# Performance work log

Measured on AMD Instinct MI355X. Metric: run time of the kernel, lower is better.

The kernel has to match this reference:

```python
import jax, jax.numpy as jnp
import numpy as np

IN_DIM = 256
QK_DIM = IN_DIM // 8


def setup_inputs() -> dict:
    key = jax.random.key(0)
    ks = jax.random.split(key, 7)
    B, C, H, W = 4, IN_DIM, 64, 64
    s = 0.05
    return {
        "x": jax.random.normal(ks[0], (B, C, H, W), dtype=jnp.float32),
        "Wq": jax.random.normal(ks[1], (QK_DIM, C), dtype=jnp.float32) * s,
        "bq": jnp.zeros((QK_DIM,), dtype=jnp.float32),
        "Wk": jax.random.normal(ks[2], (QK_DIM, C), dtype=jnp.float32) * s,
        "bk": jnp.zeros((QK_DIM,), dtype=jnp.float32),
        "Wv": jax.random.normal(ks[3], (C, C), dtype=jnp.float32) * s,
        "bv": jnp.zeros((C,), dtype=jnp.float32),
        "gamma": jnp.zeros((1,), dtype=jnp.float32),
    }


def reference(x, Wq, bq, Wk, bk, Wv, bv, gamma):
    B, C, H, W = x.shape
    N = H * W
    xf = x.reshape(B, C, N)  # [B, C, N]
    # 1x1 convs are channel matmuls
    q = jnp.einsum('oc,bcn->bno', Wq, xf) + bq  # [B, N, Cqk]
    k = jnp.einsum('oc,bcn->bon', Wk, xf) + bk[None, :, None]  # [B, Cqk, N]
    energy = jnp.einsum('bno,bom->bnm', q, k)  # [B, N, N]
    attn = jax.nn.softmax(energy, axis=-1)
    v = jnp.einsum('oc,bcn->bon', Wv, xf) + bv[None, :, None]  # [B, C, N]
    # torch: out = bmm(v, attn^T) -> out[b,c,m] = sum_n v[b,c,n]*attn[m,n]
    out = jnp.einsum('bcn,bmn->bcm', v, attn)
    out = out.reshape(B, C, H, W)
    return gamma[0] * out + x
```

## Files before the change

### kernel.cpp

```cpp
#include <hip/hip_runtime.h>
#include <hip/hip_bf16.h>
#include <cstddef>

#define NB  4
#define NC  256
#define NN  4096
#define DQK 32
#define MT  64
#define JT  64
#define NIT (NN / JT)
#define XS2 264

typedef __attribute__((ext_vector_type(8))) short short8;
typedef __attribute__((ext_vector_type(4))) float f32x4;

#define MFMA16(a, b, c) __builtin_amdgcn_mfma_f32_16x16x32_bf16((a), (b), (c), 0, 0, 0)

__device__ inline unsigned pk2bf(float a, float b) {
  __hip_bfloat162 h = __float22bfloat162_rn(make_float2(a, b));
  unsigned u;
  __builtin_memcpy(&u, &h, 4);
  return u;
}

__device__ inline void gl16(const void* g, void* s) {
  __builtin_amdgcn_global_load_lds(
      (const __attribute__((address_space(1))) void*)g,
      (__attribute__((address_space(3))) void*)s, 16, 0, 0);
}

template <int N>
__device__ inline void bar_vm() {
  asm volatile("s_waitcnt lgkmcnt(0)" ::: "memory");
  asm volatile("s_waitcnt vmcnt(%0)" ::"n"(N) : "memory");
  __builtin_amdgcn_s_barrier();
  asm volatile("" ::: "memory");
}

__global__ __launch_bounds__(256) void wcvt_kernel(
    const float* __restrict__ Wq, const float* __restrict__ Wk,
    const float* __restrict__ Wv, __hip_bfloat16* __restrict__ W16) {
  const int id4 = (blockIdx.x * 256 + threadIdx.x) * 4;
  const int row = id4 >> 8, col = id4 & 255;
  const float* src = (row < 32) ? Wq + row * 256
                   : (row < 64) ? Wk + (row - 32) * 256
                                : Wv + (row - 64) * 256;
  float4 vv = *(const float4*)(src + col);
  *(uint2*)(W16 + id4) = make_uint2(pk2bf(vv.x, vv.y), pk2bf(vv.z, vv.w));
}

__global__ __launch_bounds__(256, 4) void proj_kernel(
    const float* __restrict__ x, const __hip_bfloat16* __restrict__ W16,
    const float* __restrict__ bq, const float* __restrict__ bk,
    const float* __restrict__ bv, __hip_bfloat16* __restrict__ q,
    __hip_bfloat16* __restrict__ kT, __hip_bfloat16* __restrict__ v) {
  __shared__ __hip_bfloat16 Xs[32 * XS2];
  const int t = threadIdx.x;
  const int b = blockIdx.y, n0 = blockIdx.x * 32;
  const int w = __builtin_amdgcn_readfirstlane(t >> 6);
  const int ln = t & 15, quad = (t & 63) >> 4;
  const int sn = t & 31, scg = t >> 5;

  const float* xsrc = x + (size_t)b * NC * NN + n0 + sn;
#pragma unroll
  for (int g = 0; g < 4; ++g) {
    float xr[8];
#pragma unroll
    for (int i = 0; i < 8; ++i)
      xr[i] = xsrc[(size_t)(g * 64 + scg * 8 + i) * NN];
    uint4 pw;
    pw.x = pk2bf(xr[0], xr[1]);
    pw.y = pk2bf(xr[2], xr[3]);
    pw.z = pk2bf(xr[4], xr[5]);
    pw.w = pk2bf(xr[6], xr[7]);
    *(uint4*)&Xs[sn * XS2 + g * 64 + scg * 8] = pw;
  }
  __syncthreads();

  f32x4 zero4 = {0.f, 0.f, 0.f, 0.f};
  f32x4 acc[5][2];
#pragma unroll
  for (int i = 0; i < 5; ++i)
#pragma unroll
    for (int j = 0; j < 2; ++j) acc[i][j] = zero4;

  const __hip_bfloat16* wbase = W16 + (size_t)(w * 80 + ln) * NC + quad * 8;
  short8 afc[5], afn[5];
#pragma unroll
  for (int ot = 0; ot < 5; ++ot)
    afc[ot] = *(const short8*)(wbase + (size_t)ot * 16 * NC);

#pragma unroll 1
  for (int k0 = 0; k0 < NC; k0 += 32) {
    const int kn = k0 + 32;
    if (kn < NC) {
#pragma unroll
      for (int ot = 0; ot < 5; ++ot)
        afn[ot] = *(const short8*)(wbase + (size_t)ot * 16 * NC + kn);
    }
    short8 bfr[2];
#pragma unroll
    for (int nt = 0; nt < 2; ++nt)
      bfr[nt] = *(const short8*)&Xs[(nt * 16 + ln) * XS2 + k0 + quad * 8];
#pragma unroll
    for (int ot = 0; ot < 5; ++ot)
#pragma unroll
      for (int nt = 0; nt < 2; ++nt)
        acc[ot][nt] = MFMA16(afc[ot], bfr[nt], acc[ot][nt]);
#pragma unroll
    for (int ot = 0; ot < 5; ++ot) afc[ot] = afn[ot];
  }

#pragma unroll
  for (int ot = 0; ot < 5; ++ot) {
    const int gbase = w * 80 + ot * 16;
    if (gbase < 32) {
#pragma unroll
      for (int nt = 0; nt < 2; ++nt)
#pragma unroll
        for (int r = 0; r < 4; ++r) {
          const int row = gbase + quad * 4 + r;
          q[((size_t)b * NN + n0 + nt * 16 + ln) * DQK + row] =
              __hip_bfloat16(acc[ot][nt][r] + bq[row]);
        }
    } else if (gbase < 64) {
#pragma unroll
      for (int nt = 0; nt < 2; ++nt)
#pragma unroll
        for (int r = 0; r < 4; ++r) {
          const int row = gbase - 32 + quad * 4 + r;
          kT[((size_t)b * NN + n0 + nt * 16 + ln) * DQK + row] =
              __hip_bfloat16(acc[ot][nt][r] + bk[row]);
        }
    } else {
#pragma unroll
      for (int nt = 0; nt < 2; ++nt)
#pragma unroll
        for (int r = 0; r < 4; ++r) {
          const int c = gbase - 64 + quad * 4 + r;
          v[((size_t)b * NC + c) * NN + n0 + nt * 16 + ln] =
              __hip_bfloat16(acc[ot][nt][r] + bv[c]);
        }
    }
  }
}

__global__ __launch_bounds__(512, 2) void flash_kernel(
    const __hip_bfloat16* __restrict__ q, const __hip_bfloat16* __restrict__ kt,
    const __hip_bfloat16* __restrict__ v, const float* __restrict__ x,
    const float* __restrict__ gamma, float* __restrict__ out) {
  __shared__ __align__(16) __hip_bfloat16 Vs[4][NC * JT];
  __shared__ __align__(16) __hip_bfloat16 Ks[3][JT * DQK];
  __shared__ __align__(16) __hip_bfloat16 Ps[2][MT * JT];
  __shared__ float lrow[MT];

  const int t  = threadIdx.x;
  const int bi = blockIdx.x;
  const int b  = (bi & 7) >> 1;
  const int m0 = (((bi & 1) * 32) + (bi >> 3)) * MT;

  const int w    = __builtin_amdgcn_readfirstlane(t >> 6);
  const int l    = t & 63;
  const int ln   = t & 15;
  const int quad = (t & 63) >> 4;

  const __hip_bfloat16* kb_base = kt + (size_t)b * NN * DQK;
  const __hip_bfloat16* v_base  = v + (size_t)b * NC * NN;

  size_t voff[4];
#pragma unroll
  for (int k = 0; k < 4; ++k)
    voff[k] = (size_t)((w * 4 + k) * 8 + (l >> 3)) * NN +
              (((l & 7) ^ ((l >> 3) & 7)) * 8);
  const size_t koff = (size_t)(w * 16 + (l >> 2)) * DQK +
                      (((l & 3) ^ ((l >> 2) & 3)) * 8);

#pragma unroll
  for (int j = 0; j < 2; ++j) {
#pragma unroll
    for (int k = 0; k < 4; ++k)
      gl16(v_base + voff[k] + (size_t)j * JT, &Vs[j][(w * 4 + k) * 512]);
    if (w < 4)
      gl16(kb_base + koff + (size_t)j * JT * DQK, &Ks[j][w * 512]);
  }

  if (w < 4) {
    bar_vm<5>();
    const short8 qa =
        *(const short8*)(q + ((size_t)b * NN + m0 + w * 16 + ln) * DQK + quad * 8);
    float lreg = 0.f;
    const f32x4 zero4 = {0.f, 0.f, 0.f, 0.f};
    const int m = w * 16 + ln;

    for (int it = 0; it < NIT; ++it) {
      const bool more = (it + 2 < NIT);
      if (more) {
        const size_t jn = (size_t)(it + 2) * JT;
#pragma unroll
        for (int k = 0; k < 4; ++k)
          gl16(v_base + voff[k] + jn, &Vs[(it + 2) & 3][(w * 4 + k) * 512]);
        gl16(kb_base + koff + jn * DQK, &Ks[(it + 2) % 3][w * 512]);
      }

      short8 kb[4];
#pragma unroll
      for (int jt = 0; jt < 4; ++jt)
        kb[jt] = *(const short8*)&Ks[it % 3][(jt * 16 + ln) * DQK +
                                             ((quad ^ (ln & 3)) * 8)];
      f32x4 st[4];
      __builtin_amdgcn_s_setprio(1);
#pragma unroll
      for (int jt = 0; jt < 4; ++jt) st[jt] = MFMA16(kb[jt], qa, zero4);
      __builtin_amdgcn_s_setprio(0);

      char* pbase = (char*)&Ps[it & 1][0] + m * (JT * 2);
#pragma unroll
      for (int jt = 0; jt < 4; ++jt) {
        const float e0 = __expf(st[jt][0]), e1 = __expf(st[jt][1]);
        const float e2 = __expf(st[jt][2]), e3 = __expf(st[jt][3]);
        lreg += (e0 + e1) + (e2 + e3);
        *(uint2*)(pbase + ((jt * 32 + quad * 8) ^ ((m & 7) << 4))) =
            make_uint2(pk2bf(e0, e1), pk2bf(e2, e3));
      }
      if (more) bar_vm<5>(); else bar_vm<0>();
    }
    lreg += __shfl_xor(lreg, 16);
    lreg += __shfl_xor(lreg, 32);
    if (quad == 0) lrow[m] = lreg;
    __syncthreads();
  } else {
    bar_vm<8>();
    const int c0 = (w - 4) * 64;
    const f32x4 zero4 = {0.f, 0.f, 0.f, 0.f};
    f32x4 acc[4][4];
#pragma unroll
    for (int ct = 0; ct < 4; ++ct)
#pragma unroll
      for (int mt = 0; mt < 4; ++mt) acc[ct][mt] = zero4;

    for (int it = 0; it < NIT; ++it) {
      const bool more = (it + 2 < NIT);
      if (more) {
        const size_t jn = (size_t)(it + 2) * JT;
#pragma unroll
        for (int k = 0; k < 4; ++k)
          gl16(v_base + voff[k] + jn, &Vs[(it + 2) & 3][(w * 4 + k) * 512]);
      }
      if (it > 0) {
        const char* vbb = (const char*)&Vs[(it - 1) & 3][0];
        const char* pbb = (const char*)&Ps[(it - 1) & 1][0];
        short8 va[4][2];
#pragma unroll
        for (int ct = 0; ct < 4; ++ct)
#pragma unroll
          for (int ks = 0; ks < 2; ++ks)
            va[ct][ks] = *(const short8*)(vbb +
                (size_t)(c0 + ct * 16 + ln) * (JT * 2) +
                (((ks * 4 + quad) ^ (ln & 7)) * 16));
#pragma unroll
        for (int ks = 0; ks < 2; ++ks) {
          short8 pb[4];
#pragma unroll
          for (int mt = 0; mt < 4; ++mt)
            pb[mt] = *(const short8*)(pbb + (size_t)(mt * 16 + ln) * (JT * 2) +
                                      ((ks * 64 + quad * 16) ^ ((ln & 7) << 4)));
          __builtin_amdgcn_s_setprio(1);
#pragma unroll
          for (int ct = 0; ct < 4; ++ct)
#pragma unroll
            for (int mt = 0; mt < 4; ++mt)
              acc[ct][mt] = MFMA16(va[ct][ks], pb[mt], acc[ct][mt]);
          __builtin_amdgcn_s_setprio(0);
        }
      }
      if (more) bar_vm<8>(); else bar_vm<0>();
    }

    {
      const char* vbb = (const char*)&Vs[(NIT - 1) & 3][0];
      const char* pbb = (const char*)&Ps[(NIT - 1) & 1][0];
      short8 va[4][2];
#pragma unroll
      for (int ct = 0; ct < 4; ++ct)
#pragma unroll
        for (int ks = 0; ks < 2; ++ks)
          va[ct][ks] = *(const short8*)(vbb +
              (size_t)(c0 + ct * 16 + ln) * (JT * 2) +
              (((ks * 4 + quad) ^ (ln & 7)) * 16));
#pragma unroll
      for (int ks = 0; ks < 2; ++ks) {
        short8 pb[4];
#pragma unroll
        for (int mt = 0; mt < 4; ++mt)
          pb[mt] = *(const short8*)(pbb + (size_t)(mt * 16 + ln) * (JT * 2) +
                                    ((ks * 64 + quad * 16) ^ ((ln & 7) << 4)));
        __builtin_amdgcn_s_setprio(1);
#pragma unroll
        for (int ct = 0; ct < 4; ++ct)
#pragma unroll
          for (int mt = 0; mt < 4; ++mt)
            acc[ct][mt] = MFMA16(va[ct][ks], pb[mt], acc[ct][mt]);
        __builtin_amdgcn_s_setprio(0);
      }
    }
    __syncthreads();

    const float g0 = gamma[0];
    float li[4];
#pragma unroll
    for (int mt = 0; mt < 4; ++mt) li[mt] = 1.f / lrow[mt * 16 + ln];
#pragma unroll
    for (int ct = 0; ct < 4; ++ct)
#pragma unroll
      for (int r = 0; r < 4; ++r) {
        const int c = c0 + ct * 16 + quad * 4 + r;
        const float* xr = x + ((size_t)b * NC + c) * NN + m0;
        float* orow = out + ((size_t)b * NC + c) * NN + m0;
#pragma unroll
        for (int mt = 0; mt < 4; ++mt) {
          const int m = mt * 16 + ln;
          orow[m] = g0 * (acc[ct][mt][r] * li[mt]) + xr[m];
        }
      }
  }
}

extern "C" void kernel_launch(void* const* d_in, const int* in_sizes, int n_in,
                              void* d_out, int out_size, void* d_ws, size_t ws_size,
                              hipStream_t stream) {
  const float* x     = (const float*)d_in[0];
  const float* Wq    = (const float*)d_in[1];
  const float* bq    = (const float*)d_in[2];
  const float* Wk    = (const float*)d_in[3];
  const float* bk    = (const float*)d_in[4];
  const float* Wv    = (const float*)d_in[5];
  const float* bv    = (const float*)d_in[6];
  const float* gamma = (const float*)d_in[7];
  float* out = (float*)d_out;

  char* wsp = (char*)d_ws;
  __hip_bfloat16* W16 = (__hip_bfloat16*)wsp;  wsp += (size_t)320 * NC * 2;
  __hip_bfloat16* q   = (__hip_bfloat16*)wsp;  wsp += (size_t)NB * NN * DQK * 2;
  __hip_bfloat16* kT  = (__hip_bfloat16*)wsp;  wsp += (size_t)NB * NN * DQK * 2;
  __hip_bfloat16* v   = (__hip_bfloat16*)wsp;

  wcvt_kernel<<<dim3(80), dim3(256), 0, stream>>>(Wq, Wk, Wv, W16);
  proj_kernel<<<dim3(NN / 32, NB), dim3(256), 0, stream>>>(x, W16, bq, bk, bv, q, kT, v);
  flash_kernel<<<dim3(NB * NN / MT), dim3(512), 0, stream>>>(q, kT, v, x, gamma, out);
}
```

Before: 162.7 us.

## Replace producer/consumer warp specialization with symmetric split-K over key halves

Instead of 4 waves computing QK^T/exp and 4 waves doing the PV matmul, all 8 waves now do both: each wave owns a channel quarter and one half of each 64-key tile. Partial PV accumulators from the two key halves are reduced through shared memory (reusing the V buffer) at the end, and the row sums are combined from two halves. This is meant to remove the idle imbalance of the specialized wave roles and spread the exp work across all waves. The cost is an extra cross-wave reduction, a duplicated small QK^T MFMA per wave pair, and different barrier counts per wave group.

```diff
diff --git a/kernel.cpp b/kernel.cpp
--- a/kernel.cpp
+++ b/kernel.cpp
@@ -151,8 +151,8 @@
     const float* __restrict__ gamma, float* __restrict__ out) {
   __shared__ __align__(16) __hip_bfloat16 Vs[4][NC * JT];
   __shared__ __align__(16) __hip_bfloat16 Ks[3][JT * DQK];
-  __shared__ __align__(16) __hip_bfloat16 Ps[2][MT * JT];
-  __shared__ float lrow[MT];
+  __shared__ __align__(16) __hip_bfloat16 Ps[2][2][MT * 32];
+  __shared__ float lrow[2][MT];
 
   const int t  = threadIdx.x;
   const int bi = blockIdx.x;
@@ -163,6 +163,8 @@
   const int l    = t & 63;
   const int ln   = t & 15;
   const int quad = (t & 63) >> 4;
+  const int cq   = w & 3;
+  const int jh   = w >> 2;
 
   const __hip_bfloat16* kb_base = kt + (size_t)b * NN * DQK;
   const __hip_bfloat16* v_base  = v + (size_t)b * NC * NN;
@@ -172,7 +174,7 @@
   for (int k = 0; k < 4; ++k)
     voff[k] = (size_t)((w * 4 + k) * 8 + (l >> 3)) * NN +
               (((l & 7) ^ ((l >> 3) & 7)) * 8);
-  const size_t koff = (size_t)(w * 16 + (l >> 2)) * DQK +
+  const size_t koff = (size_t)(cq * 16 + (l >> 2)) * DQK +
                       (((l & 3) ^ ((l >> 2) & 3)) * 8);
 
 #pragma unroll
@@ -180,146 +182,142 @@
 #pragma unroll
     for (int k = 0; k < 4; ++k)
       gl16(v_base + voff[k] + (size_t)j * JT, &Vs[j][(w * 4 + k) * 512]);
-    if (w < 4)
-      gl16(kb_base + koff + (size_t)j * JT * DQK, &Ks[j][w * 512]);
-  }
-
-  if (w < 4) {
-    bar_vm<5>();
-    const short8 qa =
-        *(const short8*)(q + ((size_t)b * NN + m0 + w * 16 + ln) * DQK + quad * 8);
-    float lreg = 0.f;
-    const f32x4 zero4 = {0.f, 0.f, 0.f, 0.f};
-    const int m = w * 16 + ln;
-
-    for (int it = 0; it < NIT; ++it) {
-      const bool more = (it + 2 < NIT);
-      if (more) {
-        const size_t jn = (size_t)(it + 2) * JT;
-#pragma unroll
-        for (int k = 0; k < 4; ++k)
-          gl16(v_base + voff[k] + jn, &Vs[(it + 2) & 3][(w * 4 + k) * 512]);
-        gl16(kb_base + koff + jn * DQK, &Ks[(it + 2) % 3][w * 512]);
-      }
-
-      short8 kb[4];
-#pragma unroll
-      for (int jt = 0; jt < 4; ++jt)
-        kb[jt] = *(const short8*)&Ks[it % 3][(jt * 16 + ln) * DQK +
-                                             ((quad ^ (ln & 3)) * 8)];
-      f32x4 st[4];
+    if (jh == 0)
+      gl16(kb_base + koff + (size_t)j * JT * DQK, &Ks[j][cq * 512]);
+  }
+  if (jh == 0) bar_vm<5>(); else bar_vm<4>();
+
+  const short8 qa =
+      *(const short8*)(q + ((size_t)b * NN + m0 + cq * 16 + ln) * DQK + quad * 8);
+  const f32x4 zero4 = {0.f, 0.f, 0.f, 0.f};
+  float lreg = 0.f;
+  const int m  = cq * 16 + ln;
+  const int fp = (ln >> 1) & 3;
+  f32x4 acc[4][4];
+#pragma unroll
+  for (int ct = 0; ct < 4; ++ct)
+#pragma unroll
+    for (int mt = 0; mt < 4; ++mt) acc[ct][mt] = zero4;
+
+  for (int it = 0; it < NIT; ++it) {
+    const bool more = (it + 2 < NIT);
+    if (more) {
+      const size_t jn = (size_t)(it + 2) * JT;
+#pragma unroll
+      for (int k = 0; k < 4; ++k)
+        gl16(v_base + voff[k] + jn, &Vs[(it + 2) & 3][(w * 4 + k) * 512]);
+      if (jh == 0)
+        gl16(kb_base + koff + jn * DQK, &Ks[(it + 2) % 3][cq * 512]);
+    }
+
+    short8 kb[2];
+#pragma unroll
+    for (int jt = 0; jt < 2; ++jt) {
+      const int row = jh * 32 + jt * 16 + ln;
+      kb[jt] = *(const short8*)&Ks[it % 3][row * DQK + ((quad ^ (ln & 3)) * 8)];
+    }
+    f32x4 st[2];
+    __builtin_amdgcn_s_setprio(1);
+#pragma unroll
+    for (int jt = 0; jt < 2; ++jt) st[jt] = MFMA16(kb[jt], qa, zero4);
+    __builtin_amdgcn_s_setprio(0);
+
+    char* prow = (char*)&Ps[it & 1][jh][0] + m * 64;
+#pragma unroll
+    for (int jt = 0; jt < 2; ++jt) {
+      const float e0 = __expf(st[jt][0]), e1 = __expf(st[jt][1]);
+      const float e2 = __expf(st[jt][2]), e3 = __expf(st[jt][3]);
+      lreg += (e0 + e1) + (e2 + e3);
+      *(uint2*)(prow + (((jt * 2 + (quad >> 1)) ^ fp) * 16) + (quad & 1) * 8) =
+          make_uint2(pk2bf(e0, e1), pk2bf(e2, e3));
+    }
+
+    if (it > 0) {
+      const char* vbb = (const char*)&Vs[(it - 1) & 3][0];
+      const char* pbb = (const char*)&Ps[(it - 1) & 1][jh][0];
+      short8 va[4], pb[4];
+#pragma unroll
+      for (int ct = 0; ct < 4; ++ct)
+        va[ct] = *(const short8*)(vbb + (size_t)(cq * 64 + ct * 16 + ln) * 128 +
+                                  (((jh * 4 + quad) ^ (ln & 7)) * 16));
+#pragma unroll
+      for (int mt = 0; mt < 4; ++mt)
+        pb[mt] = *(const short8*)(pbb + (size_t)(mt * 16 + ln) * 64 +
+                                  ((quad ^ fp) * 16));
       __builtin_amdgcn_s_setprio(1);
 #pragma unroll
-      for (int jt = 0; jt < 4; ++jt) st[jt] = MFMA16(kb[jt], qa, zero4);
+      for (int ct = 0; ct < 4; ++ct)
+#pragma unroll
+        for (int mt = 0; mt < 4; ++mt)
+          acc[ct][mt] = MFMA16(va[ct], pb[mt], acc[ct][mt]);
       __builtin_amdgcn_s_setprio(0);
-
-      char* pbase = (char*)&Ps[it & 1][0] + m * (JT * 2);
-#pragma unroll
-      for (int jt = 0; jt < 4; ++jt) {
-        const float e0 = __expf(st[jt][0]), e1 = __expf(st[jt][1]);
-        const float e2 = __expf(st[jt][2]), e3 = __expf(st[jt][3]);
-        lreg += (e0 + e1) + (e2 + e3);
-        *(uint2*)(pbase + ((jt * 32 + quad * 8) ^ ((m & 7) << 4))) =
-            make_uint2(pk2bf(e0, e1), pk2bf(e2, e3));
-      }
-      if (more) bar_vm<5>(); else bar_vm<0>();
-    }
-    lreg += __shfl_xor(lreg, 16);
-    lreg += __shfl_xor(lreg, 32);
-    if (quad == 0) lrow[m] = lreg;
-    __syncthreads();
-  } else {
-    bar_vm<8>();
-    const int c0 = (w - 4) * 64;
-    const f32x4 zero4 = {0.f, 0.f, 0.f, 0.f};
-    f32x4 acc[4][4];
-#pragma unroll
-    for (int ct = 0; ct < 4; ++ct)
-#pragma unroll
-      for (int mt = 0; mt < 4; ++mt) acc[ct][mt] = zero4;
-
-    for (int it = 0; it < NIT; ++it) {
-      const bool more = (it + 2 < NIT);
-      if (more) {
-        const size_t jn = (size_t)(it + 2) * JT;
-#pragma unroll
-        for (int k = 0; k < 4; ++k)
-          gl16(v_base + voff[k] + jn, &Vs[(it + 2) & 3][(w * 4 + k) * 512]);
-      }
-      if (it > 0) {
-        const char* vbb = (const char*)&Vs[(it - 1) & 3][0];
-        const char* pbb = (const char*)&Ps[(it - 1) & 1][0];
-        short8 va[4][2];
-#pragma unroll
-        for (int ct = 0; ct < 4; ++ct)
-#pragma unroll
-          for (int ks = 0; ks < 2; ++ks)
-            va[ct][ks] = *(const short8*)(vbb +
-                (size_t)(c0 + ct * 16 + ln) * (JT * 2) +
-                (((ks * 4 + quad) ^ (ln & 7)) * 16));
-#pragma unroll
-        for (int ks = 0; ks < 2; ++ks) {
-          short8 pb[4];
-#pragma unroll
-          for (int mt = 0; mt < 4; ++mt)
-            pb[mt] = *(const short8*)(pbb + (size_t)(mt * 16 + ln) * (JT * 2) +
-                                      ((ks * 64 + quad * 16) ^ ((ln & 7) << 4)));
-          __builtin_amdgcn_s_setprio(1);
-#pragma unroll
-          for (int ct = 0; ct < 4; ++ct)
-#pragma unroll
-            for (int mt = 0; mt < 4; ++mt)
-              acc[ct][mt] = MFMA16(va[ct][ks], pb[mt], acc[ct][mt]);
-          __builtin_amdgcn_s_setprio(0);
-        }
-      }
-      if (more) bar_vm<8>(); else bar_vm<0>();
-    }
-
-    {
-      const char* vbb = (const char*)&Vs[(NIT - 1) & 3][0];
-      const char* pbb = (const char*)&Ps[(NIT - 1) & 1][0];
-      short8 va[4][2];
-#pragma unroll
-      for (int ct = 0; ct < 4; ++ct)
-#pragma unroll
-        for (int ks = 0; ks < 2; ++ks)
-          va[ct][ks] = *(const short8*)(vbb +
-              (size_t)(c0 + ct * 16 + ln) * (JT * 2) +
-              (((ks * 4 + quad) ^ (ln & 7)) * 16));
-#pragma unroll
-      for (int ks = 0; ks < 2; ++ks) {
-        short8 pb[4];
-#pragma unroll
-        for (int mt = 0; mt < 4; ++mt)
-          pb[mt] = *(const short8*)(pbb + (size_t)(mt * 16 + ln) * (JT * 2) +
-                                    ((ks * 64 + quad * 16) ^ ((ln & 7) << 4)));
-        __builtin_amdgcn_s_setprio(1);
-#pragma unroll
-        for (int ct = 0; ct < 4; ++ct)
-#pragma unroll
-          for (int mt = 0; mt < 4; ++mt)
-            acc[ct][mt] = MFMA16(va[ct][ks], pb[mt], acc[ct][mt]);
-        __builtin_amdgcn_s_setprio(0);
-      }
-    }
-    __syncthreads();
+    }
+
+    if (more) { if (jh == 0) bar_vm<5>(); else bar_vm<4>(); }
+    else      bar_vm<0>();
+  }
+
+  {
+    const char* vbb = (const char*)&Vs[(NIT - 1) & 3][0];
+    const char* pbb = (const char*)&Ps[(NIT - 1) & 1][jh][0];
+    short8 va[4], pb[4];
+#pragma unroll
+    for (int ct = 0; ct < 4; ++ct)
+      va[ct] = *(const short8*)(vbb + (size_t)(cq * 64 + ct * 16 + ln) * 128 +
+                                (((jh * 4 + quad) ^ (ln & 7)) * 16));
+#pragma unroll
+    for (int mt = 0; mt < 4; ++mt)
+      pb[mt] = *(const short8*)(pbb + (size_t)(mt * 16 + ln) * 64 +
+                                ((quad ^ fp) * 16));
+#pragma unroll
+    for (int ct = 0; ct < 4; ++ct)
+#pragma unroll
+      for (int mt = 0; mt < 4; ++mt)
+        acc[ct][mt] = MFMA16(va[ct], pb[mt], acc[ct][mt]);
+  }
+
+  lreg += __shfl_xor(lreg, 16);
+  lreg += __shfl_xor(lreg, 32);
+  if (quad == 0) lrow[jh][m] = lreg;
+  __syncthreads();
+
+  float* abuf = (float*)&Vs[0][0];
+  if (jh == 1) {
+#pragma unroll
+    for (int ct = 0; ct < 4; ++ct)
+#pragma unroll
+      for (int mt = 0; mt < 4; ++mt)
+        *(f32x4*)(abuf + (size_t)cq * 64 * 72 + (mt * 16 + ln) * 72 +
+                  ct * 16 + quad * 4) = acc[ct][mt];
+  }
+  __syncthreads();
+
+  if (jh == 0) {
+#pragma unroll
+    for (int ct = 0; ct < 4; ++ct)
+#pragma unroll
+      for (int mt = 0; mt < 4; ++mt)
+        acc[ct][mt] += *(const f32x4*)(abuf + (size_t)cq * 64 * 72 +
+                                       (mt * 16 + ln) * 72 + ct * 16 + quad * 4);
 
     const float g0 = gamma[0];
     float li[4];
 #pragma unroll
-    for (int mt = 0; mt < 4; ++mt) li[mt] = 1.f / lrow[mt * 16 + ln];
+    for (int mt = 0; mt < 4; ++mt) {
+      const int mm = mt * 16 + ln;
+      li[mt] = 1.f / (lrow[0][mm] + lrow[1][mm]);
+    }
 #pragma unroll
     for (int ct = 0; ct < 4; ++ct)
 #pragma unroll
       for (int r = 0; r < 4; ++r) {
-        const int c = c0 + ct * 16 + quad * 4 + r;
+        const int c = cq * 64 + ct * 16 + quad * 4 + r;
         const float* xr = x + ((size_t)b * NC + c) * NN + m0;
         float* orow = out + ((size_t)b * NC + c) * NN + m0;
 #pragma unroll
         for (int mt = 0; mt < 4; ++mt) {
-          const int m = mt * 16 + ln;
-          orow[m] = g0 * (acc[ct][mt][r] * li[mt]) + xr[m];
+          const int mm = mt * 16 + ln;
+          orow[mm] = g0 * (acc[ct][mt][r] * li[mt]) + xr[mm];
         }
       }
   }
```

Measured after the change: 169.8 us. +4.4%, slower.
